# Performance work log

Hardware: AMD Instinct MI355X
Metric: run time of the kernel (lower is better)

## Reference

```python
import jax, jax.numpy as jnp
import numpy as np
import math


def setup_inputs() -> dict:
    key = jax.random.key(0)
    ks = jax.random.split(key, 10)
    B, N, C, heads = 16, 1024, 256, 8
    nW = 4
    ANGLE_BINS = 5
    inner = C  # dim_head*heads == dim
    return {
        "x": jax.random.normal(ks[0], (B, N, C), jnp.float32),
        "mask": jax.random.normal(ks[1], (nW, N, N), jnp.float32),
        "affine_matrix": jax.random.normal(ks[2], (B, 2, 3), jnp.float32),
        "Wq": jax.random.normal(ks[3], (C, inner), jnp.float32) * (C ** -0.5),
        "bq": jnp.zeros((inner,), jnp.float32),
        "Wkv": jax.random.normal(ks[4], (C, 2 * inner), jnp.float32) * (C ** -0.5),
        "bkv": jnp.zeros((2 * inner,), jnp.float32),
        "Wp": jax.random.normal(ks[5], (C, C), jnp.float32) * (C ** -0.5),
        "bp": jnp.zeros((C,), jnp.float32),
        "angle_table": jnp.ones((ANGLE_BINS, heads), jnp.float32),
        "H": 32,
        "W": 32,
    }


def reference(x, mask, affine_matrix, Wq, bq, Wkv, bkv, Wp, bp, angle_table, H, W):
    B, N, C = x.shape
    heads = angle_table.shape[1]
    hd = C // heads
    scale = hd ** -0.5

    # qkv projections (torch Linear -> x @ W + b with W stored as (in, out))
    q = (x @ Wq + bq).reshape(B, N, heads, hd).transpose(0, 2, 1, 3)      # (B,h,N,d)
    kv = (x @ Wkv + bkv).reshape(B, N, 2, heads, hd).transpose(2, 0, 3, 1, 4)
    k, v = kv[0], kv[1]                                                    # (B,h,N,d)

    attn = jnp.einsum('bhqd,bhkd->bhqk', q * scale, k)                     # (B,h,N,N)

    # angle bias: per-query multiplicative bias in (1,2)
    grid_y, grid_x = jnp.meshgrid(jnp.arange(H), jnp.arange(W), indexing='ij')
    coords = jnp.stack([grid_x.reshape(-1), grid_y.reshape(-1)], -1).astype(jnp.float32)  # (N,2)
    center = jnp.array([W / 2.0, H / 2.0], jnp.float32)
    ego = jnp.einsum('bij,j->bi', affine_matrix[:, :2, :2], center) + affine_matrix[:, :2, 2]  # (B,2)
    rel = coords[None, :, :] - ego[:, None, :]                             # (B,N,2)
    ang = jnp.arctan2(rel[..., 1], rel[..., 0])
    bins = (((ang + math.pi) / (2.0 * math.pi)) * (angle_table.shape[0] - 1)).astype(jnp.int32)
    bias = 1.0 + jax.nn.sigmoid(angle_table[bins])                         # (B,N,h)
    attn = attn * bias.transpose(0, 2, 1)[..., None]                       # broadcast over keys

    # additive window mask then softmax
    nW = mask.shape[0]
    attn = attn.reshape(B // nW, nW, heads, N, N) + mask[None, :, None]
    attn = jax.nn.softmax(attn.reshape(B, heads, N, N), axis=-1)

    out = jnp.einsum('bhqk,bhkd->bhqd', attn, v).transpose(0, 2, 1, 3).reshape(B, N, C)
    return out @ Wp + bp
```

## Files before the change

kernel.cpp:

```cpp
#include <hip/hip_runtime.h>
#include <hip/hip_bf16.h>
#include <math.h>

#define BB 16
#define NTOK 1024
#define CDIM 256
#define HEADS 8
#define HD 32
#define LOG2E 1.4426950408889634f
#define PSHIFT 18.0f

typedef __attribute__((ext_vector_type(8))) _Float16 half8;
typedef __attribute__((ext_vector_type(8))) unsigned short u16x8;
typedef __attribute__((ext_vector_type(4))) unsigned int u32x4;
typedef __attribute__((ext_vector_type(4))) float f32x4;

__device__ __forceinline__ unsigned short f2h(float f) {
  _Float16 h = (_Float16)f;
  return __builtin_bit_cast(unsigned short, h);
}
__device__ __forceinline__ half8 ldh8(const unsigned short* p) {
  return *reinterpret_cast<const half8*>(p);
}
__device__ __forceinline__ void gl_lds16(const unsigned short* g,
                                         unsigned short* l) {
  __builtin_amdgcn_global_load_lds(
      (const __attribute__((address_space(1))) unsigned int*)g,
      (__attribute__((address_space(3))) unsigned int*)l, 16, 0, 0);
}

__global__ __launch_bounds__(256) void cvt_x(const float* __restrict__ X,
                                             unsigned short* __restrict__ x16) {
  size_t base = ((size_t)blockIdx.x * 256 + threadIdx.x) * 8;
  float4 a = *(const float4*)(X + base);
  float4 b = *(const float4*)(X + base + 4);
  u16x8 o = {f2h(a.x), f2h(a.y), f2h(a.z), f2h(a.w),
             f2h(b.x), f2h(b.y), f2h(b.z), f2h(b.w)};
  *(u16x8*)(x16 + base) = o;
}

__global__ __launch_bounds__(256) void cvt_w(
    const float* __restrict__ Wq, const float* __restrict__ Wkv,
    const float* __restrict__ Wp, unsigned short* __restrict__ wt16,
    unsigned short* __restrict__ wp16) {
  int idx = blockIdx.x * 256 + threadIdx.x;
  float val; size_t dst; bool isp = false;
  if (idx < 65536) {
    int k = idx >> 8, n = idx & 255;
    val = Wq[idx]; dst = (size_t)n * 256 + k;
  } else if (idx < 196608) {
    int i2 = idx - 65536;
    int k = i2 >> 9, n2 = i2 & 511;
    val = Wkv[i2]; dst = (size_t)(256 + n2) * 256 + k;
  } else {
    int i3 = idx - 196608;
    int k = i3 >> 8, n = i3 & 255;
    val = Wp[i3]; dst = (size_t)n * 256 + k; isp = true;
  }
  unsigned short h = f2h(val);
  if (isp) wp16[dst] = h; else wt16[dst] = h;
}

__global__ __launch_bounds__(256) void bias_kernel(
    const float* __restrict__ affine, const float* __restrict__ atab,
    float* __restrict__ bias) {
  int idx = blockIdx.x * 256 + threadIdx.x;
  if (idx >= BB * NTOK) return;
  int b = idx >> 10, n = idx & (NTOK - 1);
  float cx = (float)(n & 31);
  float cy = (float)(n >> 5);
  const float* A = affine + b * 6;
  float egx = fmaf(A[0], 16.f, fmaf(A[1], 16.f, A[2]));
  float egy = fmaf(A[3], 16.f, fmaf(A[4], 16.f, A[5]));
  float ang = atan2f(cy - egy, cx - egx);
  float t = (ang + 3.14159265358979323846f) *
            (1.f / (2.f * 3.14159265358979323846f)) * 4.f;
  int bin = (int)t;
  bin = bin < 0 ? 0 : (bin > 4 ? 4 : bin);
  for (int h = 0; h < HEADS; ++h) {
    float a = atab[bin * HEADS + h];
    float s = 1.f / (1.f + __expf(-a));
    bias[((size_t)b * HEADS + h) * NTOK + n] = 1.f + s;
  }
}

__global__ __launch_bounds__(256) void mask_prepF(const float* __restrict__ m,
                                                  float* __restrict__ mF) {
  int idx = blockIdx.x * 256 + threadIdx.x;
  int b4 = idx >> 18;
  int rem = idx & 262143;
  int q = rem >> 8;
  int k = (rem & 255) * 4;
  float4 v = *(const float4*)(m + ((size_t)b4 * NTOK + q) * NTOK + k);
  float4 o = {fmaf(v.x, LOG2E, -PSHIFT), fmaf(v.y, LOG2E, -PSHIFT),
              fmaf(v.z, LOG2E, -PSHIFT), fmaf(v.w, LOG2E, -PSHIFT)};
  int kt = k >> 6, hf = (k >> 5) & 1, a = (k & 31) >> 2;
  size_t base = ((size_t)((b4 * 16 + kt) * 4 + hf * 2)) * 16384 + q * 16 + a * 2;
  float2 e = {o.x, o.z};
  float2 d = {o.y, o.w};
  *(float2*)(mF + base) = e;
  *(float2*)(mF + base + 16384) = d;
}

__global__ __launch_bounds__(512, 4) void gemm_qkv16(
    const unsigned short* __restrict__ x16, const unsigned short* __restrict__ wt16,
    const float* __restrict__ bq, const float* __restrict__ bkv,
    const float* __restrict__ bias, unsigned short* __restrict__ q16,
    unsigned short* __restrict__ k16, unsigned short* __restrict__ vt16) {
  __shared__ __align__(16) unsigned short SM[16384];
  unsigned short* Xs = SM;
  unsigned short* Ws = SM + 8192;
  int tid = threadIdx.x;
  int w = tid >> 6, l = tid & 63;
  int row16 = l & 15, grp = l >> 4;
  int bid = blockIdx.x;
  int xcd = bid & 7, local = bid >> 3;
  int jb = local % 6, mb = xcd * 16 + local / 6;
  int j0 = jb * 128, m0 = mb * 128;
  int wm = w >> 1, wn = w & 1;

  auto stg = [&](int nb, int kt) {
    int k0s = kt * 32;
    int row = w * 16 + (l >> 2);
    int ge = (((l & 3) * 16) ^ ((row & 3) << 4)) >> 1;
    gl_lds16(x16 + (size_t)(m0 + row) * 256 + k0s + ge, Xs + nb * 4096 + w * 512);
    gl_lds16(wt16 + (size_t)(j0 + row) * 256 + k0s + ge, Ws + nb * 4096 + w * 512);
  };
  auto off16 = [&](int row, int g) {
    return row * 32 + ((((g * 16) ^ ((row & 3) << 4))) >> 1);
  };

  stg(0, 0);
  __syncthreads();

  f32x4 acc[2][4];
#pragma unroll
  for (int i = 0; i < 2; ++i)
#pragma unroll
    for (int c = 0; c < 4; ++c) acc[i][c] = (f32x4){0.f, 0.f, 0.f, 0.f};

  for (int kt = 0; kt < 8; ++kt) {
    int cur = kt & 1;
    if (kt < 7) stg(cur ^ 1, kt + 1);
    half8 a0 = ldh8(Xs + cur * 4096 + off16(wm * 32 + row16, grp));
    half8 a1 = ldh8(Xs + cur * 4096 + off16(wm * 32 + 16 + row16, grp));
#pragma unroll
    for (int c = 0; c < 4; ++c) {
      half8 bh = ldh8(Ws + cur * 4096 + off16(wn * 64 + c * 16 + row16, grp));
      acc[0][c] = __builtin_amdgcn_mfma_f32_16x16x32_f16(a0, bh, acc[0][c], 0, 0, 0);
      acc[1][c] = __builtin_amdgcn_mfma_f32_16x16x32_f16(a1, bh, acc[1][c], 0, 0, 0);
    }
    __syncthreads();
  }

  const float scaleq = 0.17677669529663687f * LOG2E;
  int half_mine = wm >> 1;
  for (int half = 0; half < 2; ++half) {
    if (half_mine == half) {
#pragma unroll
      for (int i = 0; i < 2; ++i) {
#pragma unroll
        for (int c = 0; c < 4; ++c) {
          int col = wn * 64 + c * 16 + row16;
          int jg = j0 + col;
#pragma unroll
          for (int r = 0; r < 4; ++r) {
            int rowl = (wm & 1) * 32 + i * 16 + grp * 4 + r;
            int m = m0 + half * 64 + rowl;
            int b = m >> 10, n = m & (NTOK - 1);
            float val = acc[i][c][r];
            unsigned short o;
            if (jb < 2)
              o = f2h((val + bq[jg]) * scaleq *
                      bias[((size_t)b * HEADS + (jg >> 5)) * NTOK + n]);
            else
              o = f2h(val + bkv[jg - CDIM]);
            SM[rowl * 136 + col] = o;
          }
        }
      }
    }
    __syncthreads();
    if (jb < 4) {
#pragma unroll
      for (int it = 0; it < 2; ++it) {
        int lin = it * 512 + tid;
        int rowb = lin >> 4, oct = lin & 15;
        u16x8 v = *(const u16x8*)&SM[rowb * 136 + oct * 8];
        int m = m0 + half * 64 + rowb;
        int b = m >> 10, n = m & (NTOK - 1);
        int jg = j0 + oct * 8;
        unsigned short* dst; int h, d;
        if (jb < 2) { h = jg >> 5; d = jg & 31; dst = q16; }
        else { int c2 = jg - CDIM; h = c2 >> 5; d = c2 & 31; dst = k16; }
        *(u16x8*)(dst + (((size_t)b * HEADS + h) * NTOK + n) * HD + d) = v;
      }
    } else {
#pragma unroll
      for (int it = 0; it < 2; ++it) {
        int lin = it * 512 + tid;
        int noct = lin >> 7, jl = lin & 127;
        u16x8 v;
#pragma unroll
        for (int e = 0; e < 8; ++e) v[e] = SM[(noct * 8 + e) * 136 + jl];
        int c3 = j0 + jl - 2 * CDIM;
        int h = c3 >> 5, d = c3 & 31;
        int n0 = m0 + half * 64 + noct * 8;
        int b = n0 >> 10, nn = n0 & (NTOK - 1);
        *(u16x8*)(vt16 + (((size_t)b * HEADS + h) * HD + d) * NTOK + nn) = v;
      }
    }
    __syncthreads();
  }
}

__global__ __launch_bounds__(512, 8) void attn16(
    const unsigned short* __restrict__ q16, const unsigned short* __restrict__ k16,
    const unsigned short* __restrict__ vt16, const float* __restrict__ maskF,
    unsigned short* __restrict__ ao16) {
  __shared__ __align__(16) unsigned short KT[2][2048];
  __shared__ __align__(16) unsigned short VT[2][2048];

  int tid = threadIdx.x;
  int w = tid >> 6, l = tid & 63;
  int row16 = l & 15, grp = l >> 4;
  int bid = blockIdx.x;
  int qt = bid & 7, h = (bid >> 3) & 7, b = bid >> 6;
  int q0 = qt * 128;
  int bh = b * HEADS + h;

  size_t qidx = (((size_t)bh * NTOK) + q0 + w * 16 + row16) * HD + grp * 8;
  half8 bq16 = ldh8(q16 + qidx);

  const float* mFb = maskF + (size_t)(b & 3) * 64 * 16384 +
                     (q0 + w * 16 + row16) * 16 + grp * 4;

  f32x4 accd[2];
  accd[0] = (f32x4){0.f, 0.f, 0.f, 0.f};
  accd[1] = (f32x4){0.f, 0.f, 0.f, 0.f};
  float lsum = 0.f;

  auto stage = [&](int nbuf, int kt2) {
    int k0n = kt2 * 64;
    if (w < 4) {
      int r = w * 16 + (l >> 2);
      int key = ((r >> 5) << 5) + 2 * (r & 15) + ((r >> 4) & 1);
      int gd = (((l & 3) * 16) ^ ((r & 3) << 4)) >> 1;
      gl_lds16(k16 + (((size_t)bh * NTOK) + k0n + key) * HD + gd,
               &KT[nbuf][w * 16 * 32]);
    } else {
      int sub = w - 4;
      int dl = sub * 8 + (l >> 3);
      int gk = (((l & 7) * 16) ^ ((dl & 7) << 4)) >> 1;
      gl_lds16(vt16 + ((size_t)bh * HD + dl) * NTOK + k0n + gk,
               &VT[nbuf][sub * 8 * 64]);
    }
  };

  stage(0, 0);
  __syncthreads();

  for (int kt = 0; kt < 16; ++kt) {
    int cur = kt & 1;
    if (kt < 15) stage(cur ^ 1, kt + 1);

    f32x4 mC[4];
#pragma unroll
    for (int f = 0; f < 4; ++f)
      mC[f] = *(const f32x4*)(mFb + (size_t)(kt * 4 + f) * 16384);

#pragma unroll
    for (int hf = 0; hf < 2; ++hf) {
      f32x4 s[2];
#pragma unroll
      for (int fp = 0; fp < 2; ++fp) {
        int f = hf * 2 + fp;
        int kl = f * 16 + row16;
        int cb = (grp * 16) ^ ((kl & 3) << 4);
        half8 kf = ldh8(&KT[cur][kl * 32 + (cb >> 1)]);
        s[fp] = __builtin_amdgcn_mfma_f32_16x16x32_f16(kf, bq16,
                                                       mC[f], 0, 0, 0);
      }
      f32x4 e0, e1;
#pragma unroll
      for (int r = 0; r < 4; ++r) {
        e0[r] = __builtin_amdgcn_exp2f(s[0][r]);
        e1[r] = __builtin_amdgcn_exp2f(s[1][r]);
      }
      lsum += ((e0[0] + e1[0]) + (e0[1] + e1[1])) +
              ((e0[2] + e1[2]) + (e0[3] + e1[3]));
      u32x4 pk;
#pragma unroll
      for (int r = 0; r < 4; ++r)
        pk[r] = __builtin_bit_cast(unsigned,
                                   __builtin_amdgcn_cvt_pkrtz(e0[r], e1[r]));
      half8 pa = __builtin_bit_cast(half8, pk);
#pragma unroll
      for (int df = 0; df < 2; ++df) {
        int dl = df * 16 + row16;
        int cb = (hf * 64 + grp * 16) ^ ((dl & 7) << 4);
        half8 v = ldh8(&VT[cur][dl * 64 + (cb >> 1)]);
        accd[df] = __builtin_amdgcn_mfma_f32_16x16x32_f16(pa, v, accd[df], 0, 0, 0);
      }
    }
    __syncthreads();
  }

  lsum += __shfl_xor(lsum, 16);
  lsum += __shfl_xor(lsum, 32);
#pragma unroll
  for (int r = 0; r < 4; ++r) {
    float lr = __shfl(lsum, grp * 4 + r, 16);
    float inv = 1.f / lr;
    int qrow = q0 + w * 16 + grp * 4 + r;
    size_t obase = ((size_t)b * NTOK + qrow) * CDIM + h * HD;
    ao16[obase + row16] = f2h(accd[0][r] * inv);
    ao16[obase + 16 + row16] = f2h(accd[1][r] * inv);
  }
}

__global__ __launch_bounds__(512, 4) void gemm_out16(
    const unsigned short* __restrict__ a16, const unsigned short* __restrict__ wp16,
    const float* __restrict__ bp, float* __restrict__ out) {
  __shared__ __align__(16) unsigned short SM[16384];
  unsigned short* Xs = SM;
  unsigned short* Ws = SM + 8192;
  int tid = threadIdx.x;
  int w = tid >> 6, l = tid & 63;
  int row16 = l & 15, grp = l >> 4;
  int bid = blockIdx.x;
  int xcd = bid & 7, local = bid >> 3;
  int jb = local & 1, mb = xcd * 16 + (local >> 1);
  int j0 = jb * 128, m0 = mb * 128;
  int wm = w >> 1, wn = w & 1;

  auto stg = [&](int nb, int kt) {
    int k0s = kt * 32;
    int row = w * 16 + (l >> 2);
    int ge = (((l & 3) * 16) ^ ((row & 3) << 4)) >> 1;
    gl_lds16(a16 + (size_t)(m0 + row) * 256 + k0s + ge, Xs + nb * 4096 + w * 512);
    gl_lds16(wp16 + (size_t)(j0 + row) * 256 + k0s + ge, Ws + nb * 4096 + w * 512);
  };
  auto off16 = [&](int row, int g) {
    return row * 32 + ((((g * 16) ^ ((row & 3) << 4))) >> 1);
  };

  stg(0, 0);
  __syncthreads();

  f32x4 acc[2][4];
#pragma unroll
  for (int i = 0; i < 2; ++i)
#pragma unroll
    for (int c = 0; c < 4; ++c) acc[i][c] = (f32x4){0.f, 0.f, 0.f, 0.f};

  for (int kt = 0; kt < 8; ++kt) {
    int cur = kt & 1;
    if (kt < 7) stg(cur ^ 1, kt + 1);
    half8 a0 = ldh8(Xs + cur * 4096 + off16(wm * 32 + row16, grp));
    half8 a1 = ldh8(Xs + cur * 4096 + off16(wm * 32 + 16 + row16, grp));
#pragma unroll
    for (int c = 0; c < 4; ++c) {
      half8 bh = ldh8(Ws + cur * 4096 + off16(wn * 64 + c * 16 + row16, grp));
      acc[0][c] = __builtin_amdgcn_mfma_f32_16x16x32_f16(a0, bh, acc[0][c], 0, 0, 0);
      acc[1][c] = __builtin_amdgcn_mfma_f32_16x16x32_f16(a1, bh, acc[1][c], 0, 0, 0);
    }
    __syncthreads();
  }

#pragma unroll
  for (int i = 0; i < 2; ++i) {
    int ng = m0 + wm * 32 + i * 16 + grp * 4;
#pragma unroll
    for (int c = 0; c < 4; ++c) {
      int jg = j0 + wn * 64 + c * 16 + row16;
      float bias = bp[jg];
#pragma unroll
      for (int r = 0; r < 4; ++r) {
        out[(size_t)(ng + r) * CDIM + jg] = acc[i][c][r] + bias;
      }
    }
  }
}

extern "C" void kernel_launch(void* const* d_in, const int* in_sizes, int n_in,
                              void* d_out, int out_size, void* d_ws,
                              size_t ws_size, hipStream_t stream) {
  const float* x = (const float*)d_in[0];
  const float* mask = (const float*)d_in[1];
  const float* affine = (const float*)d_in[2];
  const float* Wq = (const float*)d_in[3];
  const float* bq = (const float*)d_in[4];
  const float* Wkv = (const float*)d_in[5];
  const float* bkv = (const float*)d_in[6];
  const float* Wp = (const float*)d_in[7];
  const float* bp = (const float*)d_in[8];
  const float* atab = (const float*)d_in[9];
  float* out = (float*)d_out;

  const size_t bhnd = (size_t)BB * HEADS * NTOK * HD;
  unsigned short* q16 = (unsigned short*)d_ws;
  unsigned short* k16 = q16 + bhnd;
  unsigned short* vt16 = k16 + bhnd;
  unsigned short* x16 = vt16 + bhnd;
  unsigned short* wt16 = x16 + bhnd;
  unsigned short* wp16 = wt16 + 768 * 256;
  float* bias = (float*)(wp16 + 256 * 256);
  float* maskF = bias + (size_t)BB * HEADS * NTOK;

  cvt_x<<<2048, 256, 0, stream>>>(x, x16);
  cvt_w<<<1024, 256, 0, stream>>>(Wq, Wkv, Wp, wt16, wp16);
  bias_kernel<<<64, 256, 0, stream>>>(affine, atab, bias);
  mask_prepF<<<4096, 256, 0, stream>>>(mask, maskF);
  gemm_qkv16<<<768, 512, 0, stream>>>(x16, wt16, bq, bkv, bias, q16, k16, vt16);
  attn16<<<1024, 512, 0, stream>>>(q16, k16, vt16, maskF, x16);
  gemm_out16<<<256, 512, 0, stream>>>(x16, wp16, bp, out);
}
```

Baseline: 100.4 us.

## Restructure attention blocks to share mask tiles across four heads per block

The attention kernel is reorganised so each block covers 4 heads × 64 queries of one batch (each wave owning 32 queries of one head), with 32-key tiles staged per head. The grid is halved and the block-to-work mapping is changed so that blocks using the same window mask slice run on the same XCD. Mask-tile loads from L2 are meant to be reused more, and each wave now issues two query blocks per K/V fragment load. The mask layout in mask_prepF changes to match the new 32-key tiling. In exchange there are twice as many loop iterations with a barrier in each, and occupancy drops from 8 to 4 waves-per-EU per launch bound.

New measurement: 95.96 us. -4.5%, faster.

```diff
diff --git a/kernel.cpp b/kernel.cpp
--- a/kernel.cpp
+++ b/kernel.cpp
@@ -94,8 +94,9 @@
   float4 v = *(const float4*)(m + ((size_t)b4 * NTOK + q) * NTOK + k);
   float4 o = {fmaf(v.x, LOG2E, -PSHIFT), fmaf(v.y, LOG2E, -PSHIFT),
               fmaf(v.z, LOG2E, -PSHIFT), fmaf(v.w, LOG2E, -PSHIFT)};
-  int kt = k >> 6, hf = (k >> 5) & 1, a = (k & 31) >> 2;
-  size_t base = ((size_t)((b4 * 16 + kt) * 4 + hf * 2)) * 16384 + q * 16 + a * 2;
+  int kt = k >> 5;
+  int m0 = (k & 31) >> 1;
+  size_t base = ((size_t)(b4 * 64 + kt * 2)) * 16384 + q * 16 + m0;
   float2 e = {o.x, o.z};
   float2 d = {o.y, o.w};
   *(float2*)(mF + base) = e;
@@ -214,108 +215,114 @@
   }
 }
 
-__global__ __launch_bounds__(512, 8) void attn16(
+__global__ __launch_bounds__(512, 4) void attn16(
     const unsigned short* __restrict__ q16, const unsigned short* __restrict__ k16,
     const unsigned short* __restrict__ vt16, const float* __restrict__ maskF,
     unsigned short* __restrict__ ao16) {
-  __shared__ __align__(16) unsigned short KT[2][2048];
-  __shared__ __align__(16) unsigned short VT[2][2048];
+  __shared__ __align__(16) unsigned short KT[2][4][1024];
+  __shared__ __align__(16) unsigned short VT[2][4][1024];
 
   int tid = threadIdx.x;
   int w = tid >> 6, l = tid & 63;
   int row16 = l & 15, grp = l >> 4;
   int bid = blockIdx.x;
-  int qt = bid & 7, h = (bid >> 3) & 7, b = bid >> 6;
-  int q0 = qt * 128;
-  int bh = b * HEADS + h;
-
-  size_t qidx = (((size_t)bh * NTOK) + q0 + w * 16 + row16) * HD + grp * 8;
-  half8 bq16 = ldh8(q16 + qidx);
-
-  const float* mFb = maskF + (size_t)(b & 3) * 64 * 16384 +
-                     (q0 + w * 16 + row16) * 16 + grp * 4;
-
-  f32x4 accd[2];
-  accd[0] = (f32x4){0.f, 0.f, 0.f, 0.f};
-  accd[1] = (f32x4){0.f, 0.f, 0.f, 0.f};
-  float lsum = 0.f;
-
-  auto stage = [&](int nbuf, int kt2) {
-    int k0n = kt2 * 64;
-    if (w < 4) {
-      int r = w * 16 + (l >> 2);
-      int key = ((r >> 5) << 5) + 2 * (r & 15) + ((r >> 4) & 1);
-      int gd = (((l & 3) * 16) ^ ((r & 3) << 4)) >> 1;
-      gl_lds16(k16 + (((size_t)bh * NTOK) + k0n + key) * HD + gd,
-               &KT[nbuf][w * 16 * 32]);
-    } else {
-      int sub = w - 4;
-      int dl = sub * 8 + (l >> 3);
-      int gk = (((l & 7) * 16) ^ ((dl & 7) << 4)) >> 1;
-      gl_lds16(vt16 + ((size_t)bh * HD + dl) * NTOK + k0n + gk,
-               &VT[nbuf][sub * 8 * 64]);
-    }
+  int g = (bid >> 6) * 8 + (bid & 7);
+  int inner = (bid >> 3) & 7;
+  int qt = g >> 2, b4 = g & 3;
+  int brep = inner >> 1, hg = inner & 1;
+  int b = brep * 4 + b4;
+  int hl = w >> 1, qh = w & 1;
+  int head = hg * 4 + hl;
+  int bh = b * HEADS + head;
+  int qbase = qt * 64 + qh * 32;
+
+  half8 bq[2];
+#pragma unroll
+  for (int qb = 0; qb < 2; ++qb)
+    bq[qb] = ldh8(q16 + ((size_t)bh * NTOK + qbase + qb * 16 + row16) * HD +
+                  grp * 8);
+
+  const float* mFb = maskF + (size_t)b4 * 64 * 16384;
+
+  f32x4 acc[2][2];
+#pragma unroll
+  for (int i = 0; i < 2; ++i)
+#pragma unroll
+    for (int j = 0; j < 2; ++j) acc[i][j] = (f32x4){0.f, 0.f, 0.f, 0.f};
+  float lsum[2] = {0.f, 0.f};
+
+  auto off32 = [&](int row, int gg) {
+    return row * 32 + ((gg ^ ((row >> 1) & 3)) << 3);
+  };
+
+  auto stage = [&](int nb, int kt2) {
+    int k0n = (kt2 & 31) * 32;
+    int key = 2 * (l >> 2) + qh;
+    int sk = (l & 3) ^ ((qh * 8 + (l >> 3)) & 3);
+    gl_lds16(k16 + ((size_t)bh * NTOK + k0n + key) * HD + sk * 8,
+             &KT[nb][hl][qh * 512]);
+    int dl = qh * 16 + (l >> 2);
+    int sv = (l & 3) ^ ((qh * 8 + (l >> 3)) & 3);
+    gl_lds16(vt16 + ((size_t)bh * HD + dl) * NTOK + k0n + sv * 8,
+             &VT[nb][hl][qh * 512]);
   };
 
   stage(0, 0);
   __syncthreads();
 
-  for (int kt = 0; kt < 16; ++kt) {
+  for (int kt = 0; kt < 32; ++kt) {
     int cur = kt & 1;
-    if (kt < 15) stage(cur ^ 1, kt + 1);
-
-    f32x4 mC[4];
-#pragma unroll
-    for (int f = 0; f < 4; ++f)
-      mC[f] = *(const f32x4*)(mFb + (size_t)(kt * 4 + f) * 16384);
-
-#pragma unroll
-    for (int hf = 0; hf < 2; ++hf) {
-      f32x4 s[2];
-#pragma unroll
-      for (int fp = 0; fp < 2; ++fp) {
-        int f = hf * 2 + fp;
-        int kl = f * 16 + row16;
-        int cb = (grp * 16) ^ ((kl & 3) << 4);
-        half8 kf = ldh8(&KT[cur][kl * 32 + (cb >> 1)]);
-        s[fp] = __builtin_amdgcn_mfma_f32_16x16x32_f16(kf, bq16,
-                                                       mC[f], 0, 0, 0);
+    if (kt < 31) stage(cur ^ 1, kt + 1);
+
+    half8 kf0 = ldh8(&KT[cur][hl][off32(row16, grp)]);
+    half8 kf1 = ldh8(&KT[cur][hl][off32(16 + row16, grp)]);
+    half8 v0 = ldh8(&VT[cur][hl][off32(row16, grp)]);
+    half8 v1 = ldh8(&VT[cur][hl][off32(16 + row16, grp)]);
+
+#pragma unroll
+    for (int qb = 0; qb < 2; ++qb) {
+      const float* mp = mFb + (size_t)(kt * 2) * 16384 +
+                        (qbase + qb * 16 + row16) * 16 + grp * 4;
+      f32x4 mC0 = *(const f32x4*)mp;
+      f32x4 mC1 = *(const f32x4*)(mp + 16384);
+      f32x4 s0 = __builtin_amdgcn_mfma_f32_16x16x32_f16(kf0, bq[qb], mC0, 0, 0, 0);
+      f32x4 s1 = __builtin_amdgcn_mfma_f32_16x16x32_f16(kf1, bq[qb], mC1, 0, 0, 0);
+      f32x4 e0, e1;
+#pragma unroll
+      for (int r = 0; r < 4; ++r) {
+        e0[r] = __builtin_amdgcn_exp2f(s0[r]);
+        e1[r] = __builtin_amdgcn_exp2f(s1[r]);
       }
-      f32x4 e0, e1;
-#pragma unroll
-      for (int r = 0; r < 4; ++r) {
-        e0[r] = __builtin_amdgcn_exp2f(s[0][r]);
-        e1[r] = __builtin_amdgcn_exp2f(s[1][r]);
-      }
-      lsum += ((e0[0] + e1[0]) + (e0[1] + e1[1])) +
-              ((e0[2] + e1[2]) + (e0[3] + e1[3]));
+      lsum[qb] += ((e0[0] + e1[0]) + (e0[1] + e1[1])) +
+                  ((e0[2] + e1[2]) + (e0[3] + e1[3]));
       u32x4 pk;
 #pragma unroll
       for (int r = 0; r < 4; ++r)
         pk[r] = __builtin_bit_cast(unsigned,
                                    __builtin_amdgcn_cvt_pkrtz(e0[r], e1[r]));
       half8 pa = __builtin_bit_cast(half8, pk);
-#pragma unroll
-      for (int df = 0; df < 2; ++df) {
-        int dl = df * 16 + row16;
-        int cb = (hf * 64 + grp * 16) ^ ((dl & 7) << 4);
-        half8 v = ldh8(&VT[cur][dl * 64 + (cb >> 1)]);
-        accd[df] = __builtin_amdgcn_mfma_f32_16x16x32_f16(pa, v, accd[df], 0, 0, 0);
-      }
+      acc[qb][0] = __builtin_amdgcn_mfma_f32_16x16x32_f16(pa, v0, acc[qb][0], 0, 0, 0);
+      acc[qb][1] = __builtin_amdgcn_mfma_f32_16x16x32_f16(pa, v1, acc[qb][1], 0, 0, 0);
     }
     __syncthreads();
   }
 
-  lsum += __shfl_xor(lsum, 16);
-  lsum += __shfl_xor(lsum, 32);
-#pragma unroll
-  for (int r = 0; r < 4; ++r) {
-    float lr = __shfl(lsum, grp * 4 + r, 16);
-    float inv = 1.f / lr;
-    int qrow = q0 + w * 16 + grp * 4 + r;
-    size_t obase = ((size_t)b * NTOK + qrow) * CDIM + h * HD;
-    ao16[obase + row16] = f2h(accd[0][r] * inv);
-    ao16[obase + 16 + row16] = f2h(accd[1][r] * inv);
+#pragma unroll
+  for (int qb = 0; qb < 2; ++qb) {
+    lsum[qb] += __shfl_xor(lsum[qb], 16);
+    lsum[qb] += __shfl_xor(lsum[qb], 32);
+  }
+#pragma unroll
+  for (int qb = 0; qb < 2; ++qb) {
+#pragma unroll
+    for (int r = 0; r < 4; ++r) {
+      float lr = __shfl(lsum[qb], grp * 4 + r, 16);
+      float inv = 1.f / lr;
+      int qrow = qbase + qb * 16 + grp * 4 + r;
+      size_t obase = ((size_t)b * NTOK + qrow) * CDIM + head * HD;
+      ao16[obase + row16] = f2h(acc[qb][0][r] * inv);
+      ao16[obase + 16 + row16] = f2h(acc[qb][1][r] * inv);
+    }
   }
 }
 
@@ -413,6 +420,6 @@
   bias_kernel<<<64, 256, 0, stream>>>(affine, atab, bias);
   mask_prepF<<<4096, 256, 0, stream>>>(mask, maskF);
   gemm_qkv16<<<768, 512, 0, stream>>>(x16, wt16, bq, bkv, bias, q16, k16, vt16);
-  attn16<<<1024, 512, 0, stream>>>(q16, k16, vt16, maskF, x16);
+  attn16<<<512, 512, 0, stream>>>(q16, k16, vt16, maskF, x16);
   gemm_out16<<<256, 512, 0, stream>>>(x16, wp16, bp, out);
 }
```
